# Performance work log

Measured on AMD Instinct MI355X. Metric: run time of the kernel, lower is better.

## Reference

```python
import jax, jax.numpy as jnp
import numpy as np

V = 100000
E = 1600000
NODE_IN = 128
EDGE_IN = 50
H = 50  # all hidden/out sizes default to 50


def _linear_params(key, fan_in, fan_out):
    kw, kb = jax.random.split(key)
    bound = 1.0 / np.sqrt(fan_in)
    w = jax.random.uniform(kw, (fan_in, fan_out), jnp.float32, -bound, bound)
    b = jax.random.uniform(kb, (fan_out,), jnp.float32, -bound, bound)
    return w, b


def setup_inputs() -> dict:
    key = jax.random.key(0)
    ks = jax.random.split(key, 11)
    node_feats = jax.random.normal(ks[0], (V, NODE_IN), jnp.float32)
    edge_feats = jax.random.normal(ks[1], (E, EDGE_IN), jnp.float32)
    src = jax.random.randint(ks[2], (E,), 0, V, jnp.int32)
    dst = jax.random.randint(ks[3], (E,), 0, V, jnp.int32)
    w_n2n, b_n2n = _linear_params(ks[4], NODE_IN, H)
    w_e2n, b_e2n = _linear_params(ks[5], EDGE_IN, H)
    w_upd_n, b_upd_n = _linear_params(ks[6], 2 * H, H)
    w_l, b_l = _linear_params(ks[7], NODE_IN, H)
    w_r, b_r = _linear_params(ks[8], NODE_IN, H)
    w_e2e, b_e2e = _linear_params(ks[9], EDGE_IN, H)
    w_upd_e, b_upd_e = _linear_params(ks[10], 3 * H, H)
    return {
        "node_feats": node_feats, "edge_feats": edge_feats,
        "src": src, "dst": dst,
        "w_n2n": w_n2n, "b_n2n": b_n2n,
        "w_e2n": w_e2n, "b_e2n": b_e2n,
        "w_upd_n": w_upd_n, "b_upd_n": b_upd_n,
        "w_l": w_l, "b_l": b_l,
        "w_r": w_r, "b_r": b_r,
        "w_e2e": w_e2e, "b_e2e": b_e2e,
        "w_upd_e": w_upd_e, "b_upd_e": b_upd_e,
    }


def reference(node_feats, edge_feats, src, dst,
              w_n2n, b_n2n, w_e2n, b_e2n, w_upd_n, b_upd_n,
              w_l, b_l, w_r, b_r, w_e2e, b_e2e, w_upd_e, b_upd_e):
    relu = jax.nn.relu
    num_nodes = node_feats.shape[0]
    # node update
    node_node = relu(node_feats @ w_n2n + b_n2n)                # (V, H)
    e2n = relu(edge_feats @ w_e2n + b_e2n)                      # (E, H)
    # copy_edge + sum: scatter-sum edge messages onto destination nodes
    edge_node = jax.ops.segment_sum(e2n, dst, num_segments=num_nodes)  # (V, H)
    new_node = relu(jnp.concatenate([node_node, edge_node], axis=1) @ w_upd_n + b_upd_n)
    # edge update
    left = node_feats @ w_l + b_l                               # (V, H)
    right = node_feats @ w_r + b_r                              # (V, H)
    first = relu(left[src] + right[dst])                        # u_add_v(left, right)
    second = relu(right[src] + left[dst])                       # u_add_v(right, left)
    third = relu(edge_feats @ w_e2e + b_e2e)                    # (E, H)
    new_edge = relu(jnp.concatenate([first, second, third], axis=1) @ w_upd_e + b_upd_e)
    return new_node, new_edge
```

## Files before the change

### kernel.cpp

```cpp
#include <hip/hip_runtime.h>
#include <hip/hip_bf16.h>

typedef unsigned short u16;
typedef unsigned int   u32;

#define V_N 100000
#define E_N 1600000
#define NIN 128
#define EIN 50
#define HH  50
#define TPB 8

typedef __attribute__((ext_vector_type(8))) short bf16x8;
typedef __attribute__((ext_vector_type(4))) float f32x4;

__device__ __forceinline__ float bf2f(u16 u) {
    union { u32 i; float f; } v; v.i = ((u32)u) << 16; return v.f;
}
__device__ __forceinline__ u16 f2bf(float f) {
    union { float f; u32 i; } v; v.f = f;
    u32 x = v.i;
    return (u16)((x + 0x7fffu + ((x >> 16) & 1u)) >> 16);
}
__device__ __forceinline__ int swz(int row, int k) { return k ^ ((row & 7) << 3); }

__global__ __launch_bounds__(256) void k_lr(
    const float* __restrict__ nf,
    const float* __restrict__ w1, const float* __restrict__ b1,
    const float* __restrict__ w2, const float* __restrict__ b2,
    u16* __restrict__ left, u16* __restrict__ right)
{
    __shared__ u16 sw[2 * NIN * HH];
    __shared__ u16 sx[64 * NIN];
    __shared__ float sb[2 * HH];

    const int tid = threadIdx.x;
    for (int i = tid; i < NIN * HH; i += 256) {
        sw[i]          = f2bf(w1[i]);
        sw[NIN*HH + i] = f2bf(w2[i]);
    }
    if (tid < HH) {
        sb[tid]      = b1[tid];
        sb[HH + tid] = b2[tid];
    }
    const int row0 = blockIdx.x * 64;
    const float4* nf4 = (const float4*)nf;
    const int base4 = row0 * (NIN / 4);
    for (int i = tid; i < 64 * NIN / 4; i += 256) {
        float4 v = make_float4(0.f, 0.f, 0.f, 0.f);
        if (base4 + i < V_N * NIN / 4) v = nf4[base4 + i];
        ushort4 p;
        p.x = f2bf(v.x); p.y = f2bf(v.y); p.z = f2bf(v.z); p.w = f2bf(v.w);
        ((ushort4*)sx)[i] = p;
    }
    __syncthreads();

    for (int t = tid; t < 8 * HH; t += 256) {
        const int rt = t / HH, c = t - rt * HH;
        float a1[8], a2[8];
        #pragma unroll
        for (int j = 0; j < 8; ++j) { a1[j] = sb[c]; a2[j] = sb[HH+c]; }
        const u16* xr = &sx[rt * 8 * NIN];
        for (int k = 0; k < NIN; ++k) {
            const float wv1 = bf2f(sw[k*HH + c]);
            const float wv2 = bf2f(sw[NIN*HH + k*HH + c]);
            #pragma unroll
            for (int j = 0; j < 8; ++j) {
                const float x = bf2f(xr[j*NIN + k]);
                a1[j] = fmaf(x, wv1, a1[j]);
                a2[j] = fmaf(x, wv2, a2[j]);
            }
        }
        #pragma unroll
        for (int j = 0; j < 8; ++j) {
            const int r = row0 + rt*8 + j;
            if (r < V_N) {
                left [(size_t)r*HH + c] = f2bf(a1[j]);
                right[(size_t)r*HH + c] = f2bf(a2[j]);
            }
        }
    }
}

__global__ __launch_bounds__(256, 3) void k_edge(
    const float* __restrict__ ef,
    const int* __restrict__ src, const int* __restrict__ dst,
    const float* __restrict__ wA, const float* __restrict__ bA,
    const float* __restrict__ wB, const float* __restrict__ bB,
    const float* __restrict__ wU, const float* __restrict__ bU,
    const u16* __restrict__ left, const u16* __restrict__ right,
    float* __restrict__ edge_node_acc,
    float* __restrict__ out_edge)
{
    __shared__ __align__(16) u16 sint[64 * 192];
    __shared__ __align__(16) u16 wUt [64 * 192];
    __shared__ float sb[3 * HH];
    __shared__ int ssrc[64], sdst[64];

    const int tid  = threadIdx.x;
    const int lane = tid & 63, wv = tid >> 6;
    const int frow = lane & 15;
    const int kofs = (lane >> 4) << 3;
    const int rbase = wv*16 + ((lane >> 4) << 2);
    const int arow  = wv*16 + frow;

    {
        uint4 z = make_uint4(0,0,0,0);
        for (int i = tid; i < 64*192/8; i += 256) ((uint4*)sint)[i] = z;
    }
    for (int i = tid; i < 64*192; i += 256) {
        const int c = i / 192, kk = i - c*192;
        const int sec = kk >> 6, ko = kk & 63;
        u16 v = 0;
        if (c < 50 && ko < 50) v = f2bf(wU[(sec*50 + ko)*50 + c]);
        wUt[c*192 + swz(c, kk)] = v;
    }
    if (tid < 3*HH)
        sb[tid] = (tid < 50) ? bA[tid] : (tid < 100 ? bB[tid-50] : bU[tid-100]);

    bf16x8 bAf[2][4], bBf[2][4];
    #pragma unroll
    for (int kt = 0; kt < 2; ++kt) {
        #pragma unroll
        for (int nt = 0; nt < 4; ++nt) {
            union { bf16x8 v; u16 u[8]; } r1, r2;
            const int n = nt*16 + frow;
            #pragma unroll
            for (int j = 0; j < 8; ++j) {
                const int k = kt*32 + kofs + j;
                float v1 = 0.f, v2 = 0.f;
                if (k < 50 && n < 50) { v1 = wA[k*50 + n]; v2 = wB[k*50 + n]; }
                r1.u[j] = f2bf(v1); r2.u[j] = f2bf(v2);
            }
            bAf[kt][nt] = r1.v; bBf[kt][nt] = r2.v;
        }
    }
    __syncthreads();

    for (int tile = 0; tile < TPB; ++tile) {
        const int e0t = blockIdx.x * (64*TPB) + tile*64;

        if (tid < 64) { ssrc[tid] = src[e0t+tid]; sdst[tid] = dst[e0t+tid]; }
        __syncthreads();

        for (int t = tid; t < 64*25; t += 256) {
            const int e = t / 25, q = t - e*25, c = q*2;
            const int s = ssrc[e], d = sdst[e];
            const ushort2 ls  = *(const ushort2*)&left [(size_t)s*HH + c];
            const ushort2 rd_ = *(const ushort2*)&right[(size_t)d*HH + c];
            const ushort2 rs  = *(const ushort2*)&right[(size_t)s*HH + c];
            const ushort2 ld  = *(const ushort2*)&left [(size_t)d*HH + c];
            const u32 p1 = (u32)f2bf(fmaxf(bf2f(ls.x) + bf2f(rd_.x), 0.f))
                         | ((u32)f2bf(fmaxf(bf2f(ls.y) + bf2f(rd_.y), 0.f)) << 16);
            const u32 p2 = (u32)f2bf(fmaxf(bf2f(rs.x) + bf2f(ld.x), 0.f))
                         | ((u32)f2bf(fmaxf(bf2f(rs.y) + bf2f(ld.y), 0.f)) << 16);
            *(u32*)&sint[e*192 + swz(e, c)]      = p1;
            *(u32*)&sint[e*192 + swz(e, 64 + c)] = p2;
        }

        {
            f32x4 zf = {0.f, 0.f, 0.f, 0.f};
            f32x4 accA[4], accB[4];
            #pragma unroll
            for (int nt = 0; nt < 4; ++nt) { accA[nt] = zf; accB[nt] = zf; }
            const float* efr = ef + (size_t)(e0t + arow) * EIN;
            #pragma unroll
            for (int kt = 0; kt < 2; ++kt) {
                union { bf16x8 v; u16 u[8]; } a;
                #pragma unroll
                for (int p = 0; p < 4; ++p) {
                    const int k = kt*32 + kofs + 2*p;
                    float2 f = make_float2(0.f, 0.f);
                    if (k < 50) f = *(const float2*)&efr[k];
                    a.u[2*p]   = f2bf(f.x);
                    a.u[2*p+1] = f2bf(f.y);
                }
                #pragma unroll
                for (int nt = 0; nt < 4; ++nt) {
                    accA[nt] = __builtin_amdgcn_mfma_f32_16x16x32_bf16(a.v, bAf[kt][nt], accA[nt], 0, 0, 0);
                    accB[nt] = __builtin_amdgcn_mfma_f32_16x16x32_bf16(a.v, bBf[kt][nt], accB[nt], 0, 0, 0);
                }
            }
            #pragma unroll
            for (int nt = 0; nt < 4; ++nt) {
                const int c = nt*16 + frow;
                if (c < 50) {
                    const float ba = sb[c], bb = sb[HH + c];
                    #pragma unroll
                    for (int r = 0; r < 4; ++r) {
                        const int row = rbase + r;
                        const float v1 = fmaxf(accA[nt][r] + ba, 0.f);
                        atomicAdd(&edge_node_acc[(size_t)sdst[row]*HH + c], v1);
                        sint[row*192 + swz(row, 128 + c)] =
                            f2bf(fmaxf(accB[nt][r] + bb, 0.f));
                    }
                }
            }
        }
        __syncthreads();

        {
            f32x4 zf = {0.f, 0.f, 0.f, 0.f};
            f32x4 acc[4];
            #pragma unroll
            for (int nt = 0; nt < 4; ++nt) acc[nt] = zf;
            #pragma unroll
            for (int kt = 0; kt < 6; ++kt) {
                bf16x8 a = *(const bf16x8*)&sint[arow*192 + swz(arow, kt*32 + kofs)];
                #pragma unroll
                for (int nt = 0; nt < 4; ++nt) {
                    const int nrow = nt*16 + frow;
                    bf16x8 b = *(const bf16x8*)&wUt[nrow*192 + swz(nrow, kt*32 + kofs)];
                    acc[nt] = __builtin_amdgcn_mfma_f32_16x16x32_bf16(a, b, acc[nt], 0, 0, 0);
                }
            }
            #pragma unroll
            for (int nt = 0; nt < 4; ++nt) {
                const int c = nt*16 + frow;
                if (c < 50) {
                    const float bu = sb[2*HH + c];
                    #pragma unroll
                    for (int r = 0; r < 4; ++r) {
                        const int row = rbase + r;
                        out_edge[(size_t)(e0t + row)*HH + c] = fmaxf(acc[nt][r] + bu, 0.f);
                    }
                }
            }
        }
    }
}

__global__ __launch_bounds__(256) void k_node_upd(
    const float* __restrict__ nf,
    const float* __restrict__ w_n2n, const float* __restrict__ b_n2n,
    const float* __restrict__ wU, const float* __restrict__ bU,
    float* __restrict__ node_out )
{
    __shared__ u16 swn[NIN*HH];
    __shared__ u16 swu[2*HH*HH];
    __shared__ float sb[2*HH];
    __shared__ u16 sx[64*NIN];
    __shared__ u16 snn[64*HH];
    __shared__ float sen[64*HH];

    const int tid = threadIdx.x;
    for (int i = tid; i < NIN*HH; i += 256) swn[i] = f2bf(w_n2n[i]);
    for (int i = tid; i < 2*HH*HH; i += 256) swu[i] = f2bf(wU[i]);
    if (tid < HH) { sb[tid] = b_n2n[tid]; sb[HH + tid] = bU[tid]; }

    const int n0 = blockIdx.x * 64;
    const float4* nf4 = (const float4*)nf;
    const int base4 = n0 * (NIN / 4);
    for (int i = tid; i < 64 * NIN / 4; i += 256) {
        float4 v = make_float4(0.f, 0.f, 0.f, 0.f);
        if (base4 + i < V_N * NIN / 4) v = nf4[base4 + i];
        ushort4 p;
        p.x = f2bf(v.x); p.y = f2bf(v.y); p.z = f2bf(v.z); p.w = f2bf(v.w);
        ((ushort4*)sx)[i] = p;
    }
    for (int i = tid; i < 64*HH; i += 256) {
        const int gi = n0*HH + i;
        sen[i] = (gi < V_N*HH) ? node_out[gi] : 0.f;
    }
    __syncthreads();

    for (int t = tid; t < 8 * HH; t += 256) {
        const int rt = t / HH, c = t - rt * HH;
        float a[8];
        #pragma unroll
        for (int j = 0; j < 8; ++j) a[j] = sb[c];
        const u16* xr = &sx[rt * 8 * NIN];
        for (int k = 0; k < NIN; ++k) {
            const float w = bf2f(swn[k*HH + c]);
            #pragma unroll
            for (int j = 0; j < 8; ++j) a[j] = fmaf(bf2f(xr[j*NIN + k]), w, a[j]);
        }
        #pragma unroll
        for (int j = 0; j < 8; ++j)
            snn[(rt*8 + j)*HH + c] = f2bf(fmaxf(a[j], 0.f));
    }
    __syncthreads();

    for (int t = tid; t < 16 * HH; t += 256) {
        const int et = t / HH, c = t - et * HH;
        const int n = et * 4;
        float acc[4];
        #pragma unroll
        for (int j = 0; j < 4; ++j) acc[j] = sb[HH + c];
        for (int k = 0; k < HH; ++k) {
            const float w = bf2f(swu[k*HH + c]);
            #pragma unroll
            for (int j = 0; j < 4; ++j) acc[j] = fmaf(bf2f(snn[(n+j)*HH + k]), w, acc[j]);
        }
        for (int k = 0; k < HH; ++k) {
            const float w = bf2f(swu[(HH + k)*HH + c]);
            #pragma unroll
            for (int j = 0; j < 4; ++j) acc[j] = fmaf(sen[(n+j)*HH + k], w, acc[j]);
        }
        #pragma unroll
        for (int j = 0; j < 4; ++j) {
            const int r = n0 + n + j;
            if (r < V_N) node_out[(size_t)r*HH + c] = fmaxf(acc[j], 0.f);
        }
    }
}

extern "C" void kernel_launch(void* const* d_in, const int* in_sizes, int n_in,
                              void* d_out, int out_size, void* d_ws, size_t ws_size,
                              hipStream_t stream) {
    const float* nf    = (const float*)d_in[0];
    const float* ef    = (const float*)d_in[1];
    const int*   src   = (const int*)d_in[2];
    const int*   dst   = (const int*)d_in[3];
    const float* w_n2n = (const float*)d_in[4];  const float* b_n2n = (const float*)d_in[5];
    const float* w_e2n = (const float*)d_in[6];  const float* b_e2n = (const float*)d_in[7];
    const float* w_updn= (const float*)d_in[8];  const float* b_updn= (const float*)d_in[9];
    const float* w_l   = (const float*)d_in[10]; const float* b_l   = (const float*)d_in[11];
    const float* w_r   = (const float*)d_in[12]; const float* b_r   = (const float*)d_in[13];
    const float* w_e2e = (const float*)d_in[14]; const float* b_e2e = (const float*)d_in[15];
    const float* w_upde= (const float*)d_in[16]; const float* b_upde= (const float*)d_in[17];

    char* ws = (char*)d_ws;
    u16* left  = (u16*)ws;
    u16* right = (u16*)(ws + 10000000);

    float* out_node = (float*)d_out;
    float* out_edge = out_node + (size_t)V_N * HH;

    hipMemsetAsync(out_node, 0, (size_t)V_N * HH * sizeof(float), stream);

    k_lr<<<(V_N + 63)/64, 256, 0, stream>>>(nf, w_l, b_l, w_r, b_r, left, right);

    k_edge<<<E_N/(64*TPB), 256, 0, stream>>>(
        ef, src, dst, w_e2n, b_e2n, w_e2e, b_e2e, w_upde, b_upde,
        left, right, out_node, out_edge);

    k_node_upd<<<(V_N + 63)/64, 256, 0, stream>>>(
        nf, w_n2n, b_n2n, w_updn, b_updn, out_node);
}
```

Baseline: 1.417 ms.

## Port node-side GEMM kernels k_lr and k_node_upd to bf16 MFMA

Replaces the scalar FMA loops in the left/right projection kernel and the node-update kernel with MFMA 16x16x32 bf16 tiles over swizzled LDS layouts holding transposed, padded weights. The node-update second GEMM splits the fp32 edge_node aggregate into hi/lo bf16 parts so the bf16 MFMA keeps near-fp32 accuracy. Occupancy hints are added via launch bounds. The goal is to cut the ALU-bound time of the node kernels. It costs padding waste (112 and 64 columns for 100 and 50 outputs) and extra LDS.

```diff
diff --git a/kernel.cpp b/kernel.cpp
--- a/kernel.cpp
+++ b/kernel.cpp
@@ -24,59 +24,74 @@
 }
 __device__ __forceinline__ int swz(int row, int k) { return k ^ ((row & 7) << 3); }
 
-__global__ __launch_bounds__(256) void k_lr(
+__global__ __launch_bounds__(256, 3) void k_lr(
     const float* __restrict__ nf,
     const float* __restrict__ w1, const float* __restrict__ b1,
     const float* __restrict__ w2, const float* __restrict__ b2,
     u16* __restrict__ left, u16* __restrict__ right)
 {
-    __shared__ u16 sw[2 * NIN * HH];
-    __shared__ u16 sx[64 * NIN];
-    __shared__ float sb[2 * HH];
-
-    const int tid = threadIdx.x;
-    for (int i = tid; i < NIN * HH; i += 256) {
-        sw[i]          = f2bf(w1[i]);
-        sw[NIN*HH + i] = f2bf(w2[i]);
-    }
-    if (tid < HH) {
-        sb[tid]      = b1[tid];
-        sb[HH + tid] = b2[tid];
-    }
+    __shared__ __align__(16) u16 sxa[64 * 128];
+    __shared__ __align__(16) u16 swt[112 * 128];
+    __shared__ float sb[112];
+
+    const int tid  = threadIdx.x;
     const int row0 = blockIdx.x * 64;
+
     const float4* nf4 = (const float4*)nf;
-    const int base4 = row0 * (NIN / 4);
-    for (int i = tid; i < 64 * NIN / 4; i += 256) {
+    for (int i = tid; i < 64 * 32; i += 256) {
+        const int row = i >> 5, k4 = (i & 31) << 2;
         float4 v = make_float4(0.f, 0.f, 0.f, 0.f);
-        if (base4 + i < V_N * NIN / 4) v = nf4[base4 + i];
+        const int gr = row0 + row;
+        if (gr < V_N) v = nf4[(size_t)gr * 32 + (k4 >> 2)];
         ushort4 p;
         p.x = f2bf(v.x); p.y = f2bf(v.y); p.z = f2bf(v.z); p.w = f2bf(v.w);
-        ((ushort4*)sx)[i] = p;
-    }
+        *(ushort4*)&sxa[(row << 7) + swz(row, k4)] = p;
+    }
+    for (int i = tid; i < 112 * 128; i += 256) {
+        const int n = i >> 7, k = i & 127;
+        float v = 0.f;
+        if (n < 50)       v = w1[k*50 + n];
+        else if (n < 100) v = w2[k*50 + (n - 50)];
+        swt[(n << 7) + swz(n, k)] = f2bf(v);
+    }
+    if (tid < 112)
+        sb[tid] = (tid < 50) ? b1[tid] : (tid < 100 ? b2[tid - 50] : 0.f);
     __syncthreads();
 
-    for (int t = tid; t < 8 * HH; t += 256) {
-        const int rt = t / HH, c = t - rt * HH;
-        float a1[8], a2[8];
+    const int lane = tid & 63, wv = tid >> 6;
+    const int frow = lane & 15;
+    const int kofs = (lane >> 4) << 3;
+    const int rbase = wv*16 + ((lane >> 4) << 2);
+    const int arow  = wv*16 + frow;
+
+    f32x4 zf = {0.f, 0.f, 0.f, 0.f};
+    f32x4 acc[7];
+    #pragma unroll
+    for (int nt = 0; nt < 7; ++nt) acc[nt] = zf;
+
+    #pragma unroll
+    for (int kt = 0; kt < 4; ++kt) {
+        bf16x8 a = *(const bf16x8*)&sxa[(arow << 7) + swz(arow, kt*32 + kofs)];
         #pragma unroll
-        for (int j = 0; j < 8; ++j) { a1[j] = sb[c]; a2[j] = sb[HH+c]; }
-        const u16* xr = &sx[rt * 8 * NIN];
-        for (int k = 0; k < NIN; ++k) {
-            const float wv1 = bf2f(sw[k*HH + c]);
-            const float wv2 = bf2f(sw[NIN*HH + k*HH + c]);
-            #pragma unroll
-            for (int j = 0; j < 8; ++j) {
-                const float x = bf2f(xr[j*NIN + k]);
-                a1[j] = fmaf(x, wv1, a1[j]);
-                a2[j] = fmaf(x, wv2, a2[j]);
-            }
-        }
-        #pragma unroll
-        for (int j = 0; j < 8; ++j) {
-            const int r = row0 + rt*8 + j;
-            if (r < V_N) {
-                left [(size_t)r*HH + c] = f2bf(a1[j]);
-                right[(size_t)r*HH + c] = f2bf(a2[j]);
+        for (int nt = 0; nt < 7; ++nt) {
+            const int nrow = nt*16 + frow;
+            bf16x8 b = *(const bf16x8*)&swt[(nrow << 7) + swz(nrow, kt*32 + kofs)];
+            acc[nt] = __builtin_amdgcn_mfma_f32_16x16x32_bf16(a, b, acc[nt], 0, 0, 0);
+        }
+    }
+    #pragma unroll
+    for (int nt = 0; nt < 7; ++nt) {
+        const int g = nt*16 + frow;
+        if (g < 100) {
+            const float bias = sb[g];
+            #pragma unroll
+            for (int r = 0; r < 4; ++r) {
+                const int gr = row0 + rbase + r;
+                if (gr < V_N) {
+                    const u16 o = f2bf(acc[nt][r] + bias);
+                    if (g < 50) left [(size_t)gr*HH + g]      = o;
+                    else        right[(size_t)gr*HH + g - 50] = o;
+                }
             }
         }
     }
@@ -230,77 +245,128 @@
     }
 }
 
-__global__ __launch_bounds__(256) void k_node_upd(
+__global__ __launch_bounds__(256, 2) void k_node_upd(
     const float* __restrict__ nf,
     const float* __restrict__ w_n2n, const float* __restrict__ b_n2n,
     const float* __restrict__ wU, const float* __restrict__ bU,
     float* __restrict__ node_out )
 {
-    __shared__ u16 swn[NIN*HH];
-    __shared__ u16 swu[2*HH*HH];
-    __shared__ float sb[2*HH];
-    __shared__ u16 sx[64*NIN];
-    __shared__ u16 snn[64*HH];
-    __shared__ float sen[64*HH];
+    __shared__ __align__(16) u16 smem[64*128 + 64*128];
+    __shared__ __align__(16) u16 swu[64 * 192];
+    __shared__ float sb[128];
 
     const int tid = threadIdx.x;
-    for (int i = tid; i < NIN*HH; i += 256) swn[i] = f2bf(w_n2n[i]);
-    for (int i = tid; i < 2*HH*HH; i += 256) swu[i] = f2bf(wU[i]);
-    if (tid < HH) { sb[tid] = b_n2n[tid]; sb[HH + tid] = bU[tid]; }
-
-    const int n0 = blockIdx.x * 64;
+    const int n0  = blockIdx.x * 64;
+
     const float4* nf4 = (const float4*)nf;
-    const int base4 = n0 * (NIN / 4);
-    for (int i = tid; i < 64 * NIN / 4; i += 256) {
+    for (int i = tid; i < 64 * 32; i += 256) {
+        const int row = i >> 5, k4 = (i & 31) << 2;
         float4 v = make_float4(0.f, 0.f, 0.f, 0.f);
-        if (base4 + i < V_N * NIN / 4) v = nf4[base4 + i];
+        const int gr = n0 + row;
+        if (gr < V_N) v = nf4[(size_t)gr * 32 + (k4 >> 2)];
         ushort4 p;
         p.x = f2bf(v.x); p.y = f2bf(v.y); p.z = f2bf(v.z); p.w = f2bf(v.w);
-        ((ushort4*)sx)[i] = p;
-    }
-    for (int i = tid; i < 64*HH; i += 256) {
-        const int gi = n0*HH + i;
-        sen[i] = (gi < V_N*HH) ? node_out[gi] : 0.f;
+        *(ushort4*)&smem[(row << 7) + swz(row, k4)] = p;
+    }
+    for (int i = tid; i < 64 * 128; i += 256) {
+        const int n = i >> 7, k = i & 127;
+        const float v = (n < 50) ? w_n2n[k*50 + n] : 0.f;
+        smem[8192 + (n << 7) + swz(n, k)] = f2bf(v);
+    }
+    for (int i = tid; i < 64 * 192; i += 256) {
+        const int n = i / 192, kk = i - n*192;
+        float v = 0.f;
+        if (n < 50) {
+            if (kk < 100)      v = wU[kk*50 + n];
+            else if (kk < 150) v = wU[(kk - 50)*50 + n];
+        }
+        swu[n*192 + swz(n, kk)] = f2bf(v);
+    }
+    if (tid < 128) {
+        float v = 0.f;
+        if (tid < 50) v = b_n2n[tid];
+        else if (tid >= 64 && tid < 114) v = bU[tid - 64];
+        sb[tid] = v;
     }
     __syncthreads();
 
-    for (int t = tid; t < 8 * HH; t += 256) {
-        const int rt = t / HH, c = t - rt * HH;
-        float a[8];
+    const int lane = tid & 63, wv = tid >> 6;
+    const int frow = lane & 15;
+    const int kofs = (lane >> 4) << 3;
+    const int rbase = wv*16 + ((lane >> 4) << 2);
+    const int arow  = wv*16 + frow;
+
+    f32x4 zf = {0.f, 0.f, 0.f, 0.f};
+
+    f32x4 accB[4];
+    #pragma unroll
+    for (int nt = 0; nt < 4; ++nt) accB[nt] = zf;
+    #pragma unroll
+    for (int kt = 0; kt < 4; ++kt) {
+        bf16x8 a = *(const bf16x8*)&smem[(arow << 7) + swz(arow, kt*32 + kofs)];
         #pragma unroll
-        for (int j = 0; j < 8; ++j) a[j] = sb[c];
-        const u16* xr = &sx[rt * 8 * NIN];
-        for (int k = 0; k < NIN; ++k) {
-            const float w = bf2f(swn[k*HH + c]);
-            #pragma unroll
-            for (int j = 0; j < 8; ++j) a[j] = fmaf(bf2f(xr[j*NIN + k]), w, a[j]);
-        }
+        for (int nt = 0; nt < 4; ++nt) {
+            const int nrow = nt*16 + frow;
+            bf16x8 b = *(const bf16x8*)&smem[8192 + (nrow << 7) + swz(nrow, kt*32 + kofs)];
+            accB[nt] = __builtin_amdgcn_mfma_f32_16x16x32_bf16(a, b, accB[nt], 0, 0, 0);
+        }
+    }
+    __syncthreads();
+
+    #pragma unroll
+    for (int nt = 0; nt < 4; ++nt) {
+        const int g = nt*16 + frow;
+        if (g < 50) {
+            const float bias = sb[g];
+            #pragma unroll
+            for (int r = 0; r < 4; ++r) {
+                const int row = rbase + r;
+                smem[row*192 + swz(row, g)] = f2bf(fmaxf(accB[nt][r] + bias, 0.f));
+            }
+        }
+    }
+    for (int i = tid; i < 4096; i += 256) {
+        const int row = i >> 6, q = i & 63;
+        if (q < 50) {
+            float en = 0.f;
+            const int gr = n0 + row;
+            if (gr < V_N) en = node_out[(size_t)gr*HH + q];
+            const u16 hi = f2bf(en);
+            const u16 lo = f2bf(en - bf2f(hi));
+            smem[row*192 + swz(row,  50 + q)] = hi;
+            smem[row*192 + swz(row, 100 + q)] = lo;
+        }
+    }
+    for (int i = tid; i < 4096; i += 256) {
+        const int row = i >> 6, q = i & 63;
+        if (q < 42) smem[row*192 + swz(row, 150 + q)] = 0;
+    }
+    __syncthreads();
+
+    f32x4 accC[4];
+    #pragma unroll
+    for (int nt = 0; nt < 4; ++nt) accC[nt] = zf;
+    #pragma unroll
+    for (int kt = 0; kt < 6; ++kt) {
+        bf16x8 a = *(const bf16x8*)&smem[arow*192 + swz(arow, kt*32 + kofs)];
         #pragma unroll
-        for (int j = 0; j < 8; ++j)
-            snn[(rt*8 + j)*HH + c] = f2bf(fmaxf(a[j], 0.f));
-    }
-    __syncthreads();
-
-    for (int t = tid; t < 16 * HH; t += 256) {
-        const int et = t / HH, c = t - et * HH;
-        const int n = et * 4;
-        float acc[4];
-        #pragma unroll
-        for (int j = 0; j < 4; ++j) acc[j] = sb[HH + c];
-        for (int k = 0; k < HH; ++k) {
-            const float w = bf2f(swu[k*HH + c]);
-            #pragma unroll
-            for (int j = 0; j < 4; ++j) acc[j] = fmaf(bf2f(snn[(n+j)*HH + k]), w, acc[j]);
-        }
-        for (int k = 0; k < HH; ++k) {
-            const float w = bf2f(swu[(HH + k)*HH + c]);
-            #pragma unroll
-            for (int j = 0; j < 4; ++j) acc[j] = fmaf(sen[(n+j)*HH + k], w, acc[j]);
-        }
-        #pragma unroll
-        for (int j = 0; j < 4; ++j) {
-            const int r = n0 + n + j;
-            if (r < V_N) node_out[(size_t)r*HH + c] = fmaxf(acc[j], 0.f);
+        for (int nt = 0; nt < 4; ++nt) {
+            const int nrow = nt*16 + frow;
+            bf16x8 b = *(const bf16x8*)&swu[nrow*192 + swz(nrow, kt*32 + kofs)];
+            accC[nt] = __builtin_amdgcn_mfma_f32_16x16x32_bf16(a, b, accC[nt], 0, 0, 0);
+        }
+    }
+    #pragma unroll
+    for (int nt = 0; nt < 4; ++nt) {
+        const int g = nt*16 + frow;
+        if (g < 50) {
+            const float bias = sb[64 + g];
+            #pragma unroll
+            for (int r = 0; r < 4; ++r) {
+                const int gr = n0 + rbase + r;
+                if (gr < V_N)
+                    node_out[(size_t)gr*HH + g] = fmaxf(accC[nt][r] + bias, 0.f);
+            }
         }
     }
 }
```

Result: faster. 1.275 ms (-10.0%).
